# Kernel tuning notes

Hardware: AMD Instinct MI355X
Metric: run time of the kernel (lower is better)

Reference implementation:

```python
import jax, jax.numpy as jnp
import numpy as np

B, N, C = 8, 4096, 1024
ATT_DIM = 512
M = 64  # num_outputs


def setup_inputs() -> dict:
    key = jax.random.key(0)
    k_x, k_w, k_b, k_av = jax.random.split(key, 4)
    x = jax.random.normal(k_x, (B, N, C), dtype=jnp.float32)
    # nn.Linear(input_dim, attention_dim): weight (att, C), bias (att,)
    lim = 1.0 / np.sqrt(C)
    W = jax.random.uniform(k_w, (ATT_DIM, C), dtype=jnp.float32, minval=-lim, maxval=lim)
    b = jax.random.uniform(k_b, (ATT_DIM,), dtype=jnp.float32, minval=-lim, maxval=lim)
    # torch.rand -> uniform [0,1)
    attention_vectors = jax.random.uniform(k_av, (M, ATT_DIM), dtype=jnp.float32)
    return {"x": x, "W": W, "b": b, "attention_vectors": attention_vectors}


def reference(x, W, b, attention_vectors):
    # linear projection: (B,N,C) @ (C,att) + bias -> (B,N,att)
    scores = jnp.einsum('bnc,dc->bnd', x, W) + b
    # learned-query attention logits: (B,M,N)
    logits = jnp.einsum('bnd,md->bmn', scores, attention_vectors)
    weights = jax.nn.softmax(logits, axis=-1)
    # pool original features: (B,M,N) @ (B,N,C) -> (B,M,C)
    return jnp.einsum('bmn,bnc->bmc', weights, x)
```

## Files before the change

### kernel.cpp

```cpp
#include <hip/hip_runtime.h>
#include <hip/hip_bf16.h>

#define Bn 8
#define Nn 4096
#define Cn 1024
#define Dn 512
#define Mn 64

typedef __hip_bfloat16 bf16;
typedef __attribute__((ext_vector_type(8))) short short8;
typedef __attribute__((ext_vector_type(4))) short short4x;
typedef __attribute__((ext_vector_type(4))) float f32x4;

#define MFMA16(a, b, c) __builtin_amdgcn_mfma_f32_16x16x32_bf16((a), (b), (c), 0, 0, 0)

__device__ inline short bfbits(float f) {
  union { bf16 b; short s; } u;
  u.b = __float2bfloat16(f);
  return u.s;
}

__global__ __launch_bounds__(256) void zero_kernel(float* __restrict__ out) {
  const int i = blockIdx.x * 256 + threadIdx.x;
  ((float4*)out)[i] = (float4){0.f, 0.f, 0.f, 0.f};
}

__global__ __launch_bounds__(256) void prep_kernel(
    const float* __restrict__ W, const float* __restrict__ bias,
    const float* __restrict__ av, bf16* __restrict__ Vhi,
    bf16* __restrict__ Vlo, float* __restrict__ c0) {
  const int m = blockIdx.x;
  const int t = threadIdx.x;
  const int cl = t & 63, dg = t >> 6;
  const int c = blockIdx.y * 64 + cl;
  const float* wp = W + (size_t)(dg * 128) * Cn + c;
  const float* ap = av + m * Dn + dg * 128;
  float a0 = 0.f, a1 = 0.f, a2 = 0.f, a3 = 0.f;
#pragma unroll 8
  for (int i = 0; i < 128; i += 4) {
    a0 = fmaf(ap[i + 0], wp[(size_t)(i + 0) * Cn], a0);
    a1 = fmaf(ap[i + 1], wp[(size_t)(i + 1) * Cn], a1);
    a2 = fmaf(ap[i + 2], wp[(size_t)(i + 2) * Cn], a2);
    a3 = fmaf(ap[i + 3], wp[(size_t)(i + 3) * Cn], a3);
  }
  __shared__ float red[256];
  red[t] = (a0 + a1) + (a2 + a3);
  __syncthreads();
  const float v = red[cl] + red[cl + 64] + red[cl + 128] + red[cl + 192];
  if (dg == 0) {
    const bf16 hi = __float2bfloat16(v);
    Vhi[m * Cn + c] = hi;
    Vlo[m * Cn + c] = __float2bfloat16(v - __bfloat162float(hi));
  }
  if (blockIdx.y == 0) {
    __syncthreads();
    red[t] = av[m * Dn + t] * bias[t] + av[m * Dn + t + 256] * bias[t + 256];
    __syncthreads();
    if (t < 64) {
      float s = red[t] + red[t + 64] + red[t + 128] + red[t + 192];
#pragma unroll
      for (int off = 32; off > 0; off >>= 1) s += __shfl_down(s, off);
      if (t == 0) c0[m] = s;
    }
  }
}

__global__ __launch_bounds__(256) void logits_kernel(
    const float* __restrict__ x, const bf16* __restrict__ Vhi,
    const bf16* __restrict__ Vlo, const float* __restrict__ c0,
    float* __restrict__ logits) {
  const int n0 = blockIdx.x * 64;
  const int b = blockIdx.y;
  const int t = threadIdx.x;
  __shared__ short Xs[64][136];
  __shared__ short VsH[64][136];
  __shared__ short VsL[64][136];
  const int w = t >> 6, lane = t & 63, lr = lane & 15, q = lane >> 4;
  const ptrdiff_t dlo = Vlo - Vhi;

  int ur[4], uc[4];
  const float* xsrc[4];
  const bf16* hsrc[4];
#pragma unroll
  for (int j = 0; j < 4; ++j) {
    const int u = t + 256 * j;
    ur[j] = u >> 4;
    uc[j] = (u & 15) * 8;
    xsrc[j] = x + (size_t)(b * Nn + n0 + ur[j]) * Cn + uc[j];
    hsrc[j] = Vhi + ur[j] * Cn + uc[j];
  }

  f32x4 acc[4];
#pragma unroll
  for (int i = 0; i < 4; ++i) acc[i] = (f32x4){0.f, 0.f, 0.f, 0.f};

  float4 px0[4], px1[4];
  short8 pvh[4], pvl[4];
#pragma unroll
  for (int j = 0; j < 4; ++j) {
    px0[j] = *(const float4*)(xsrc[j]);
    px1[j] = *(const float4*)(xsrc[j] + 4);
    pvh[j] = *(const short8*)(hsrc[j]);
    pvl[j] = *(const short8*)(hsrc[j] + dlo);
  }

  for (int k0 = 0; k0 < Cn; k0 += 128) {
#pragma unroll
    for (int j = 0; j < 4; ++j) {
      short8 s;
      s[0] = bfbits(px0[j].x); s[1] = bfbits(px0[j].y);
      s[2] = bfbits(px0[j].z); s[3] = bfbits(px0[j].w);
      s[4] = bfbits(px1[j].x); s[5] = bfbits(px1[j].y);
      s[6] = bfbits(px1[j].z); s[7] = bfbits(px1[j].w);
      *(short8*)&Xs[ur[j]][uc[j]] = s;
      *(short8*)&VsH[ur[j]][uc[j]] = pvh[j];
      *(short8*)&VsL[ur[j]][uc[j]] = pvl[j];
    }
    __syncthreads();
    if (k0 + 128 < Cn) {
#pragma unroll
      for (int j = 0; j < 4; ++j) {
        px0[j] = *(const float4*)(xsrc[j] + k0 + 128);
        px1[j] = *(const float4*)(xsrc[j] + k0 + 132);
        pvh[j] = *(const short8*)(hsrc[j] + k0 + 128);
        pvl[j] = *(const short8*)(hsrc[j] + dlo + k0 + 128);
      }
    }
#pragma unroll
    for (int kk = 0; kk < 128; kk += 32) {
      const short8 a = *(const short8*)&Xs[w * 16 + lr][kk + q * 8];
#pragma unroll
      for (int mt = 0; mt < 4; ++mt) {
        acc[mt] = MFMA16(a, *(const short8*)&VsH[mt * 16 + lr][kk + q * 8], acc[mt]);
        acc[mt] = MFMA16(a, *(const short8*)&VsL[mt * 16 + lr][kk + q * 8], acc[mt]);
      }
    }
    __syncthreads();
  }
#pragma unroll
  for (int mt = 0; mt < 4; ++mt) {
    const int m = mt * 16 + lr;
    const float bb = c0[m];
    float4 o;
    o.x = acc[mt][0] + bb; o.y = acc[mt][1] + bb;
    o.z = acc[mt][2] + bb; o.w = acc[mt][3] + bb;
    *(float4*)&logits[(size_t)(b * Mn + m) * Nn + n0 + w * 16 + q * 4] = o;
  }
}

__global__ __launch_bounds__(256) void softmax_kernel(
    const float* __restrict__ logits, bf16* __restrict__ wgt) {
  const int row = blockIdx.x;
  const int t = threadIdx.x;
  const float* L = logits + (size_t)row * Nn;
  float v[16];
  float mx = -3.4e38f;
#pragma unroll
  for (int i = 0; i < 16; ++i) {
    v[i] = L[t + 256 * i];
    mx = fmaxf(mx, v[i]);
  }
#pragma unroll
  for (int off = 32; off > 0; off >>= 1) mx = fmaxf(mx, __shfl_down(mx, off));
  __shared__ float sred[4];
  if ((t & 63) == 0) sred[t >> 6] = mx;
  __syncthreads();
  mx = fmaxf(fmaxf(sred[0], sred[1]), fmaxf(sred[2], sred[3]));
  float sum = 0.f;
#pragma unroll
  for (int i = 0; i < 16; ++i) {
    v[i] = __expf(v[i] - mx);
    sum += v[i];
  }
#pragma unroll
  for (int off = 32; off > 0; off >>= 1) sum += __shfl_down(sum, off);
  __syncthreads();
  if ((t & 63) == 0) sred[t >> 6] = sum;
  __syncthreads();
  const float inv = 1.f / (sred[0] + sred[1] + sred[2] + sred[3]);
#pragma unroll
  for (int i = 0; i < 16; ++i)
    wgt[(size_t)row * Nn + t + 256 * i] = __float2bfloat16(v[i] * inv);
}

__global__ __launch_bounds__(256) void pool_kernel(
    const float* __restrict__ x, const bf16* __restrict__ wgt,
    float* __restrict__ out) {
  const int cbase = blockIdx.x * 64;
  const int b = blockIdx.y;
  const int ks = blockIdx.z;
  const int t = threadIdx.x;
  __shared__ short XT[64][136];
  const int w = t >> 6, lane = t & 63, lr = lane & 15, q = lane >> 4;
  const int mh = (w & 1) * 32, ch = (w >> 1) * 32;
  f32x4 acc[2][2];
#pragma unroll
  for (int i = 0; i < 2; ++i)
#pragma unroll
    for (int j = 0; j < 2; ++j) acc[i][j] = (f32x4){0.f, 0.f, 0.f, 0.f};

  const int h = t & 15, g = t >> 4;
  const int swz = 8 * (h & 7);
  const int swzr0 = 8 * (((ch + lr) >> 2) & 7);
  const int swzr1 = 8 * (((ch + 16 + lr) >> 2) & 7);
  const int NQ = Nn / 8;
  const int kbase = ks * NQ;
  const float* xsrc = x + (size_t)b * Nn * Cn + (size_t)(kbase + 4 * g) * Cn + cbase + 4 * h;
  const bf16* wr0 = wgt + (size_t)(b * Mn + mh + lr) * Nn + kbase;
  const bf16* wr1 = wr0 + (size_t)16 * Nn;

  float4 pf[8];
#pragma unroll
  for (int i = 0; i < 4; ++i) {
    pf[i]     = *(const float4*)(xsrc + (size_t)i * Cn);
    pf[4 + i] = *(const float4*)(xsrc + (size_t)(64 + i) * Cn);
  }

  for (int kc = 0; kc < NQ; kc += 128) {
#pragma unroll
    for (int blk = 0; blk < 2; ++blk) {
      const float4 r0 = pf[blk * 4 + 0], r1 = pf[blk * 4 + 1];
      const float4 r2 = pf[blk * 4 + 2], r3 = pf[blk * 4 + 3];
      const int kof = (blk * 64 + 4 * g) ^ swz;
      short4x v0, v1, v2, v3;
      v0[0] = bfbits(r0.x); v0[1] = bfbits(r1.x); v0[2] = bfbits(r2.x); v0[3] = bfbits(r3.x);
      v1[0] = bfbits(r0.y); v1[1] = bfbits(r1.y); v1[2] = bfbits(r2.y); v1[3] = bfbits(r3.y);
      v2[0] = bfbits(r0.z); v2[1] = bfbits(r1.z); v2[2] = bfbits(r2.z); v2[3] = bfbits(r3.z);
      v3[0] = bfbits(r0.w); v3[1] = bfbits(r1.w); v3[2] = bfbits(r2.w); v3[3] = bfbits(r3.w);
      *(short4x*)&XT[4 * h + 0][kof] = v0;
      *(short4x*)&XT[4 * h + 1][kof] = v1;
      *(short4x*)&XT[4 * h + 2][kof] = v2;
      *(short4x*)&XT[4 * h + 3][kof] = v3;
    }
    __syncthreads();
    if (kc + 128 < NQ) {
#pragma unroll
      for (int i = 0; i < 4; ++i) {
        pf[i]     = *(const float4*)(xsrc + (size_t)(kc + 128 + i) * Cn);
        pf[4 + i] = *(const float4*)(xsrc + (size_t)(kc + 192 + i) * Cn);
      }
    }
#pragma unroll
    for (int kk = 0; kk < 128; kk += 32) {
      const short8 a0 = *(const short8*)(wr0 + kc + kk + q * 8);
      const short8 a1 = *(const short8*)(wr1 + kc + kk + q * 8);
      const short8 b0 = *(const short8*)&XT[ch + lr][(kk + q * 8) ^ swzr0];
      const short8 b1 = *(const short8*)&XT[ch + 16 + lr][(kk + q * 8) ^ swzr1];
      acc[0][0] = MFMA16(a0, b0, acc[0][0]);
      acc[0][1] = MFMA16(a0, b1, acc[0][1]);
      acc[1][0] = MFMA16(a1, b0, acc[1][0]);
      acc[1][1] = MFMA16(a1, b1, acc[1][1]);
    }
    __syncthreads();
  }
  float* pout = out + (size_t)b * Mn * Cn;
#pragma unroll
  for (int mi = 0; mi < 2; ++mi)
#pragma unroll
    for (int ci = 0; ci < 2; ++ci) {
      const int m = mh + mi * 16 + q * 4;
      const int c = cbase + ch + ci * 16 + lr;
#pragma unroll
      for (int reg = 0; reg < 4; ++reg)
        atomicAdd(&pout[(size_t)(m + reg) * Cn + c], acc[mi][ci][reg]);
    }
}

extern "C" void kernel_launch(void* const* d_in, const int* in_sizes, int n_in,
                              void* d_out, int out_size, void* d_ws, size_t ws_size,
                              hipStream_t stream) {
  const float* x = (const float*)d_in[0];
  const float* W = (const float*)d_in[1];
  const float* bias = (const float*)d_in[2];
  const float* av = (const float*)d_in[3];
  float* out = (float*)d_out;
  char* ws = (char*)d_ws;

  bf16* Vhi = (bf16*)(ws + 0);
  bf16* Vlo = (bf16*)(ws + 131072);
  float* c0 = (float*)(ws + 262144);
  float* logits = (float*)(ws + 263168);
  bf16* wgt = (bf16*)(ws + 8651776);

  zero_kernel<<<(Bn * Mn * Cn) / 1024, 256, 0, stream>>>(out);
  prep_kernel<<<dim3(Mn, Cn / 64), 256, 0, stream>>>(W, bias, av, Vhi, Vlo, c0);
  logits_kernel<<<dim3(Nn / 64, Bn), 256, 0, stream>>>(x, Vhi, Vlo, c0, logits);
  softmax_kernel<<<Bn * Mn, 256, 0, stream>>>(logits, wgt);
  pool_kernel<<<dim3(Cn / 64, Bn, 8), 256, 0, stream>>>(x, wgt, out);
}
```

Before: 247.2 us.

## Fuse all stages into one cooperative persistent kernel with grid syncs

Replaces the five separate launches (zero, prep, logits, softmax, pool) with a single cooperative kernel of 256 blocks of 512 threads. Each block runs two 256-thread teams, and grid.sync separates the stages. It also prefetches the first x tile before the first grid sync and doubles the pool split-K chunk size (NQ from N/8 to N/4), so there are fewer atomic partial sums. The aim is to remove launch overhead and inter-kernel gaps. The costs are grid-wide barriers and lower parallelism in each stage, with the old multi-kernel path kept as a fallback.

```diff
diff --git a/kernel.cpp b/kernel.cpp
--- a/kernel.cpp
+++ b/kernel.cpp
@@ -1,5 +1,8 @@
 #include <hip/hip_runtime.h>
 #include <hip/hip_bf16.h>
+#include <hip/hip_cooperative_groups.h>
+
+namespace cg = cooperative_groups;
 
 #define Bn 8
 #define Nn 4096
@@ -18,6 +21,263 @@
   union { bf16 b; short s; } u;
   u.b = __float2bfloat16(f);
   return u.s;
+}
+
+union SMem {
+  struct { short Xs[2][64][136]; short VsH[2][64][136]; short VsL[2][64][136]; } pB;
+  short XT[2][64][136];
+  float red[2][256];
+  float sred[2][4];
+};
+
+__global__ __launch_bounds__(512, 2) void fused_kernel(
+    const float* __restrict__ x, const float* __restrict__ W,
+    const float* __restrict__ bias, const float* __restrict__ av,
+    float* __restrict__ out, bf16* __restrict__ Vhi, bf16* __restrict__ Vlo,
+    float* __restrict__ c0, float* __restrict__ logits, bf16* __restrict__ wgt) {
+  extern __shared__ char smraw[];
+  SMem& sm = *(SMem*)smraw;
+  const int bid = blockIdx.x;
+  const int t = threadIdx.x;
+  const int team = t >> 8, st = t & 255;
+  cg::grid_group grid = cg::this_grid();
+  const int w = st >> 6, lane = st & 63, lr = lane & 15, q = lane >> 4;
+
+  ((float4*)out)[bid * 512 + t] = (float4){0.f, 0.f, 0.f, 0.f};
+  {
+    const int cl = st & 63, dg = st >> 6;
+#pragma unroll
+    for (int i = 0; i < 2; ++i) {
+      const int u = 4 * bid + 2 * i + team;
+      const int m = u >> 4;
+      const int c = (u & 15) * 64 + cl;
+      const float* wp = W + (size_t)(dg * 128) * Cn + c;
+      const float* ap = av + m * Dn + dg * 128;
+      float a0 = 0.f, a1 = 0.f, a2 = 0.f, a3 = 0.f;
+#pragma unroll 8
+      for (int k = 0; k < 128; k += 4) {
+        a0 = fmaf(ap[k + 0], wp[(size_t)(k + 0) * Cn], a0);
+        a1 = fmaf(ap[k + 1], wp[(size_t)(k + 1) * Cn], a1);
+        a2 = fmaf(ap[k + 2], wp[(size_t)(k + 2) * Cn], a2);
+        a3 = fmaf(ap[k + 3], wp[(size_t)(k + 3) * Cn], a3);
+      }
+      sm.red[team][st] = (a0 + a1) + (a2 + a3);
+      __syncthreads();
+      const float v = sm.red[team][cl] + sm.red[team][cl + 64] +
+                      sm.red[team][cl + 128] + sm.red[team][cl + 192];
+      if (dg == 0) {
+        const bf16 hi = __float2bfloat16(v);
+        Vhi[m * Cn + c] = hi;
+        Vlo[m * Cn + c] = __float2bfloat16(v - __bfloat162float(hi));
+      }
+      __syncthreads();
+    }
+    if ((bid & 3) == 0 && t < 64) {
+      const int m = bid >> 2;
+      float s = 0.f;
+#pragma unroll
+      for (int j = 0; j < 8; ++j) s += av[m * Dn + t + 64 * j] * bias[t + 64 * j];
+#pragma unroll
+      for (int off = 32; off > 0; off >>= 1) s += __shfl_down(s, off);
+      if (t == 0) c0[m] = s;
+    }
+  }
+
+  const int tileB = 2 * bid + team;
+  const int n0 = (tileB & 63) * 64;
+  const int bB = tileB >> 6;
+  int ur[4], uc[4];
+  const float* xsrcB[4];
+  const bf16* hsrc[4];
+#pragma unroll
+  for (int j = 0; j < 4; ++j) {
+    const int u = st + 256 * j;
+    ur[j] = u >> 4;
+    uc[j] = (u & 15) * 8;
+    xsrcB[j] = x + (size_t)(bB * Nn + n0 + ur[j]) * Cn + uc[j];
+    hsrc[j] = Vhi + ur[j] * Cn + uc[j];
+  }
+  float4 px0[4], px1[4];
+#pragma unroll
+  for (int j = 0; j < 4; ++j) {
+    px0[j] = *(const float4*)(xsrcB[j]);
+    px1[j] = *(const float4*)(xsrcB[j] + 4);
+  }
+
+  grid.sync();
+
+  {
+    const ptrdiff_t dlo = Vlo - Vhi;
+    f32x4 acc[4];
+#pragma unroll
+    for (int i = 0; i < 4; ++i) acc[i] = (f32x4){0.f, 0.f, 0.f, 0.f};
+    short8 pvh[4], pvl[4];
+#pragma unroll
+    for (int j = 0; j < 4; ++j) {
+      pvh[j] = *(const short8*)(hsrc[j]);
+      pvl[j] = *(const short8*)(hsrc[j] + dlo);
+    }
+
+    for (int k0 = 0; k0 < Cn; k0 += 128) {
+#pragma unroll
+      for (int j = 0; j < 4; ++j) {
+        short8 s;
+        s[0] = bfbits(px0[j].x); s[1] = bfbits(px0[j].y);
+        s[2] = bfbits(px0[j].z); s[3] = bfbits(px0[j].w);
+        s[4] = bfbits(px1[j].x); s[5] = bfbits(px1[j].y);
+        s[6] = bfbits(px1[j].z); s[7] = bfbits(px1[j].w);
+        *(short8*)&sm.pB.Xs[team][ur[j]][uc[j]] = s;
+        *(short8*)&sm.pB.VsH[team][ur[j]][uc[j]] = pvh[j];
+        *(short8*)&sm.pB.VsL[team][ur[j]][uc[j]] = pvl[j];
+      }
+      __syncthreads();
+      if (k0 + 128 < Cn) {
+#pragma unroll
+        for (int j = 0; j < 4; ++j) {
+          px0[j] = *(const float4*)(xsrcB[j] + k0 + 128);
+          px1[j] = *(const float4*)(xsrcB[j] + k0 + 132);
+          pvh[j] = *(const short8*)(hsrc[j] + k0 + 128);
+          pvl[j] = *(const short8*)(hsrc[j] + dlo + k0 + 128);
+        }
+      }
+#pragma unroll
+      for (int kk = 0; kk < 128; kk += 32) {
+        const short8 a = *(const short8*)&sm.pB.Xs[team][w * 16 + lr][kk + q * 8];
+#pragma unroll
+        for (int mt = 0; mt < 4; ++mt) {
+          acc[mt] = MFMA16(a, *(const short8*)&sm.pB.VsH[team][mt * 16 + lr][kk + q * 8], acc[mt]);
+          acc[mt] = MFMA16(a, *(const short8*)&sm.pB.VsL[team][mt * 16 + lr][kk + q * 8], acc[mt]);
+        }
+      }
+      __syncthreads();
+    }
+#pragma unroll
+    for (int mt = 0; mt < 4; ++mt) {
+      const int m = mt * 16 + lr;
+      const float bb = c0[m];
+      float4 o;
+      o.x = acc[mt][0] + bb; o.y = acc[mt][1] + bb;
+      o.z = acc[mt][2] + bb; o.w = acc[mt][3] + bb;
+      *(float4*)&logits[(size_t)(bB * Mn + m) * Nn + n0 + w * 16 + q * 4] = o;
+    }
+  }
+
+  grid.sync();
+
+  {
+    const int row = 2 * bid + team;
+    const float* L = logits + (size_t)row * Nn;
+    float v[16];
+    float mx = -3.4e38f;
+#pragma unroll
+    for (int i = 0; i < 16; ++i) {
+      v[i] = L[st + 256 * i];
+      mx = fmaxf(mx, v[i]);
+    }
+#pragma unroll
+    for (int off = 32; off > 0; off >>= 1) mx = fmaxf(mx, __shfl_down(mx, off));
+    if ((st & 63) == 0) sm.sred[team][st >> 6] = mx;
+    __syncthreads();
+    mx = fmaxf(fmaxf(sm.sred[team][0], sm.sred[team][1]),
+               fmaxf(sm.sred[team][2], sm.sred[team][3]));
+    float sum = 0.f;
+#pragma unroll
+    for (int i = 0; i < 16; ++i) {
+      v[i] = __expf(v[i] - mx);
+      sum += v[i];
+    }
+#pragma unroll
+    for (int off = 32; off > 0; off >>= 1) sum += __shfl_down(sum, off);
+    __syncthreads();
+    if ((st & 63) == 0) sm.sred[team][st >> 6] = sum;
+    __syncthreads();
+    const float inv = 1.f / (sm.sred[team][0] + sm.sred[team][1] +
+                             sm.sred[team][2] + sm.sred[team][3]);
+#pragma unroll
+    for (int i = 0; i < 16; ++i)
+      wgt[(size_t)row * Nn + st + 256 * i] = __float2bfloat16(v[i] * inv);
+  }
+
+  grid.sync();
+
+  {
+    const int tile = 2 * bid + team;
+    const int cbase = (tile & 15) * 64;
+    const int b = (tile >> 4) & 7;
+    const int ks = tile >> 7;
+    const int mh = (w & 1) * 32, ch = (w >> 1) * 32;
+    f32x4 acc[2][2];
+#pragma unroll
+    for (int i = 0; i < 2; ++i)
+#pragma unroll
+      for (int j = 0; j < 2; ++j) acc[i][j] = (f32x4){0.f, 0.f, 0.f, 0.f};
+
+    const int h = st & 15, g = st >> 4;
+    const int swz = 8 * (h & 7);
+    const int swzr0 = 8 * (((ch + lr) >> 2) & 7);
+    const int swzr1 = 8 * (((ch + 16 + lr) >> 2) & 7);
+    const int NQ = Nn / 4;
+    const int kbase = ks * NQ;
+    const float* xsrc = x + (size_t)b * Nn * Cn + (size_t)(kbase + 4 * g) * Cn + cbase + 4 * h;
+    const bf16* wr0 = wgt + (size_t)(b * Mn + mh + lr) * Nn + kbase;
+    const bf16* wr1 = wr0 + (size_t)16 * Nn;
+
+    float4 pf[8];
+#pragma unroll
+    for (int i = 0; i < 4; ++i) {
+      pf[i]     = *(const float4*)(xsrc + (size_t)i * Cn);
+      pf[4 + i] = *(const float4*)(xsrc + (size_t)(64 + i) * Cn);
+    }
+
+    for (int kc = 0; kc < NQ; kc += 128) {
+#pragma unroll
+      for (int blk = 0; blk < 2; ++blk) {
+        const float4 r0 = pf[blk * 4 + 0], r1 = pf[blk * 4 + 1];
+        const float4 r2 = pf[blk * 4 + 2], r3 = pf[blk * 4 + 3];
+        const int kof = (blk * 64 + 4 * g) ^ swz;
+        short4x v0, v1, v2, v3;
+        v0[0] = bfbits(r0.x); v0[1] = bfbits(r1.x); v0[2] = bfbits(r2.x); v0[3] = bfbits(r3.x);
+        v1[0] = bfbits(r0.y); v1[1] = bfbits(r1.y); v1[2] = bfbits(r2.y); v1[3] = bfbits(r3.y);
+        v2[0] = bfbits(r0.z); v2[1] = bfbits(r1.z); v2[2] = bfbits(r2.z); v2[3] = bfbits(r3.z);
+        v3[0] = bfbits(r0.w); v3[1] = bfbits(r1.w); v3[2] = bfbits(r2.w); v3[3] = bfbits(r3.w);
+        *(short4x*)&sm.XT[team][4 * h + 0][kof] = v0;
+        *(short4x*)&sm.XT[team][4 * h + 1][kof] = v1;
+        *(short4x*)&sm.XT[team][4 * h + 2][kof] = v2;
+        *(short4x*)&sm.XT[team][4 * h + 3][kof] = v3;
+      }
+      __syncthreads();
+      if (kc + 128 < NQ) {
+#pragma unroll
+        for (int i = 0; i < 4; ++i) {
+          pf[i]     = *(const float4*)(xsrc + (size_t)(kc + 128 + i) * Cn);
+          pf[4 + i] = *(const float4*)(xsrc + (size_t)(kc + 192 + i) * Cn);
+        }
+      }
+#pragma unroll
+      for (int kk = 0; kk < 128; kk += 32) {
+        const short8 a0 = *(const short8*)(wr0 + kc + kk + q * 8);
+        const short8 a1 = *(const short8*)(wr1 + kc + kk + q * 8);
+        const short8 b0 = *(const short8*)&sm.XT[team][ch + lr][(kk + q * 8) ^ swzr0];
+        const short8 b1 = *(const short8*)&sm.XT[team][ch + 16 + lr][(kk + q * 8) ^ swzr1];
+        acc[0][0] = MFMA16(a0, b0, acc[0][0]);
+        acc[0][1] = MFMA16(a0, b1, acc[0][1]);
+        acc[1][0] = MFMA16(a1, b0, acc[1][0]);
+        acc[1][1] = MFMA16(a1, b1, acc[1][1]);
+      }
+      __syncthreads();
+    }
+    float* pout = out + (size_t)b * Mn * Cn;
+#pragma unroll
+    for (int mi = 0; mi < 2; ++mi)
+#pragma unroll
+      for (int ci = 0; ci < 2; ++ci) {
+        const int m = mh + mi * 16 + q * 4;
+        const int c = cbase + ch + ci * 16 + lr;
+#pragma unroll
+        for (int reg = 0; reg < 4; ++reg)
+          atomicAdd(&pout[(size_t)(m + reg) * Cn + c], acc[mi][ci][reg]);
+      }
+  }
 }
 
 __global__ __launch_bounds__(256) void zero_kernel(float* __restrict__ out) {
@@ -77,7 +337,6 @@
   __shared__ short VsL[64][136];
   const int w = t >> 6, lane = t & 63, lr = lane & 15, q = lane >> 4;
   const ptrdiff_t dlo = Vlo - Vhi;
-
   int ur[4], uc[4];
   const float* xsrc[4];
   const bf16* hsrc[4];
@@ -89,11 +348,9 @@
     xsrc[j] = x + (size_t)(b * Nn + n0 + ur[j]) * Cn + uc[j];
     hsrc[j] = Vhi + ur[j] * Cn + uc[j];
   }
-
   f32x4 acc[4];
 #pragma unroll
   for (int i = 0; i < 4; ++i) acc[i] = (f32x4){0.f, 0.f, 0.f, 0.f};
-
   float4 px0[4], px1[4];
   short8 pvh[4], pvl[4];
 #pragma unroll
@@ -103,7 +360,6 @@
     pvh[j] = *(const short8*)(hsrc[j]);
     pvl[j] = *(const short8*)(hsrc[j] + dlo);
   }
-
   for (int k0 = 0; k0 < Cn; k0 += 128) {
 #pragma unroll
     for (int j = 0; j < 4; ++j) {
@@ -198,7 +454,6 @@
   for (int i = 0; i < 2; ++i)
 #pragma unroll
     for (int j = 0; j < 2; ++j) acc[i][j] = (f32x4){0.f, 0.f, 0.f, 0.f};
-
   const int h = t & 15, g = t >> 4;
   const int swz = 8 * (h & 7);
   const int swzr0 = 8 * (((ch + lr) >> 2) & 7);
@@ -208,14 +463,12 @@
   const float* xsrc = x + (size_t)b * Nn * Cn + (size_t)(kbase + 4 * g) * Cn + cbase + 4 * h;
   const bf16* wr0 = wgt + (size_t)(b * Mn + mh + lr) * Nn + kbase;
   const bf16* wr1 = wr0 + (size_t)16 * Nn;
-
   float4 pf[8];
 #pragma unroll
   for (int i = 0; i < 4; ++i) {
     pf[i]     = *(const float4*)(xsrc + (size_t)i * Cn);
     pf[4 + i] = *(const float4*)(xsrc + (size_t)(64 + i) * Cn);
   }
-
   for (int kc = 0; kc < NQ; kc += 128) {
 #pragma unroll
     for (int blk = 0; blk < 2; ++blk) {
@@ -282,6 +535,34 @@
   float* logits = (float*)(ws + 263168);
   bf16* wgt = (bf16*)(ws + 8651776);
 
+  static int coop_ok = -1;
+  if (coop_ok < 0) {
+    coop_ok = 0;
+    (void)hipFuncSetAttribute((const void*)fused_kernel,
+                              hipFuncAttributeMaxDynamicSharedMemorySize,
+                              (int)sizeof(SMem));
+    int nb = 0;
+    hipError_t e = hipOccupancyMaxActiveBlocksPerMultiprocessor(
+        &nb, fused_kernel, 512, sizeof(SMem));
+    if (e == hipSuccess && nb >= 1) {
+      hipDeviceProp_t prop;
+      int dev = 0;
+      if (hipGetDevice(&dev) == hipSuccess &&
+          hipGetDeviceProperties(&prop, dev) == hipSuccess &&
+          (long)nb * prop.multiProcessorCount >= 256)
+        coop_ok = 1;
+    }
+  }
+
+  if (coop_ok == 1) {
+    void* args[] = {(void*)&x, (void*)&W, (void*)&bias, (void*)&av, (void*)&out,
+                    (void*)&Vhi, (void*)&Vlo, (void*)&c0, (void*)&logits, (void*)&wgt};
+    hipError_t e = hipLaunchCooperativeKernel((const void*)fused_kernel, dim3(256),
+                                              dim3(512), args, sizeof(SMem), stream);
+    if (e == hipSuccess) return;
+    coop_ok = 0;
+  }
+
   zero_kernel<<<(Bn * Mn * Cn) / 1024, 256, 0, stream>>>(out);
   prep_kernel<<<dim3(Mn, Cn / 64), 256, 0, stream>>>(W, bias, av, Vhi, Vlo, c0);
   logits_kernel<<<dim3(Nn / 64, Bn), 256, 0, stream>>>(x, Vhi, Vlo, c0, logits);
```

After: 248.4 us. No clear change (+0.5%).
